# Kernel tuning notes

Measured on AMD Instinct MI355X. Metric: run time of the kernel, lower is better.

## Reference

```python
import jax, jax.numpy as jnp
import numpy as np

H, DK, DV, CHUNK = 4, 256, 256, 32

def _silu(x):
    return x * jax.nn.sigmoid(x)

def _l2norm(x, eps=1e-6):
    return x * jax.lax.rsqrt(jnp.sum(x * x, -1, keepdims=True) + eps)

def _rmsnorm(x, w, eps=1e-5):
    return x * jax.lax.rsqrt(jnp.mean(x * x, -1, keepdims=True) + eps) * w

def _causal_dwconv(x, w):
    # x: (B, L, C), w: (C, K) -> causal depthwise conv -> (B, L, C)
    C = x.shape[-1]
    K = w.shape[-1]
    xp = jnp.pad(x, ((0, 0), (K - 1, 0), (0, 0))).transpose(0, 2, 1)  # NCH
    y = jax.lax.conv_general_dilated(xp, w[:, None, :], (1,), 'VALID',
                                     feature_group_count=C,
                                     dimension_numbers=('NCH', 'OIH', 'NCH'))
    return y.transpose(0, 2, 1)

def _fir(x, filt):
    # x: (B, L, H, D), filt: (H, D, K) depthwise causal FIR per (head, channel)
    B, L, h, d = x.shape
    y = _causal_dwconv(x.reshape(B, L, h * d), filt.reshape(h * d, -1))
    return y.reshape(B, L, h, d)

def _delta_rule_chunkwise(q, k, v, beta):
    # q,k: (B,H,L,DK); v: (B,H,L,DV); beta: (B,H,L). L % CHUNK == 0.
    b, h, L, dk = q.shape
    dv = v.shape[-1]
    n = L // CHUNK
    q = _l2norm(q)
    k = _l2norm(k)
    v = v * beta[..., None]
    k_beta = k * beta[..., None]
    rs = lambda t: t.reshape(b, h, n, CHUNK, -1)
    q, k, v, k_beta = rs(q), rs(k), rs(v), rs(k_beta)
    eye = jnp.eye(CHUNK, dtype=q.dtype)
    strict_lower = jnp.tril(jnp.ones((CHUNK, CHUNK), bool), -1)
    A = jnp.where(strict_lower, jnp.einsum('bhncd,bhnsd->bhncs', k_beta, k), 0.0)
    # The torch row-wise loop computes (I + strict_lower(K_beta K^T))^{-1}
    attn_inv = jax.scipy.linalg.solve_triangular(eye + A, jnp.broadcast_to(eye, A.shape), lower=True)
    u = attn_inv @ v       # (b,h,n,c,dv)
    w = attn_inv @ k_beta  # (b,h,n,c,dk)
    incl_lower = jnp.tril(jnp.ones((CHUNK, CHUNK), bool))

    def step(S, inp):
        q_i, k_i, u_i, w_i = inp
        attn_local = jnp.where(incl_lower, q_i @ jnp.swapaxes(k_i, -1, -2), 0.0)
        u_t = u_i - w_i @ S
        o_i = q_i @ S + attn_local @ u_t
        return S + jnp.swapaxes(k_i, -1, -2) @ u_t, o_i

    S0 = jnp.zeros((b, h, dk, dv), q.dtype)
    xs = tuple(jnp.moveaxis(t, 2, 0) for t in (q, k, u, w))
    S, out = jax.lax.scan(step, S0, xs)
    return jnp.moveaxis(out, 0, 2).reshape(b, h, L, dv), S

def _stats(x):
    # per-branch head statistics over feature dim: mean, var, abs-mean, l2-norm
    return jnp.stack([x.mean(-1), x.var(-1), jnp.abs(x).mean(-1),
                      jnp.sqrt(jnp.sum(x * x, -1))], -1)

def _forward(x, Wq, Wk, Wv, Wb, conv_q, conv_k, conv_v, fir_long, fir_short,
             W1, b1, W2, b2, log_temp, base_bias, conv_residual_logit, rms_w, Wo):
    B, L, D = x.shape
    q = _silu(_causal_dwconv(x @ Wq, conv_q)).reshape(B, L, H, DK)
    k = _silu(_causal_dwconv(x @ Wk, conv_k)).reshape(B, L, H, DK)
    v = _silu(_causal_dwconv(x @ Wv, conv_v)).reshape(B, L, H, DV)
    beta = jax.nn.sigmoid(x @ Wb)  # (B, L, H)
    delta, _S = _delta_rule_chunkwise(q.transpose(0, 2, 1, 3), k.transpose(0, 2, 1, 3),
                                      v.transpose(0, 2, 1, 3), beta.transpose(0, 2, 1))
    delta = delta.transpose(0, 2, 1, 3)  # (B, L, H, DV)
    f_short = _fir(v, fir_short)
    f_long = _fir(v, fir_long)
    stats = jnp.concatenate([_stats(f_short), _stats(f_long), _stats(delta), _stats(v)], -1)
    hidden_exp = jnp.broadcast_to(x[:, :, None, :], (B, L, H, D))
    gate_in = jnp.concatenate([hidden_exp, stats], -1)  # (B,L,H,D+16)
    h1 = jax.nn.gelu(gate_in @ W1 + b1, approximate=False)
    logits = h1 @ W2 + b2 + base_bias  # (B, L, H, 4)
    temp = jax.nn.softplus(log_temp) + 1e-4
    p = jax.nn.softmax(logits / temp[:, None], -1)
    eps = 0.05  # step 0 -> alpha = 1 -> floor = floor_start
    p = jnp.maximum(p, jnp.array([eps, eps, 0.0, 0.0], p.dtype))
    p = p / jnp.sum(p, -1, keepdims=True)
    o = (p[..., 0:1] * f_short + p[..., 1:2] * f_long +
         p[..., 2:3] * delta + p[..., 3:4] * v)
    o = o + 0.5 * jax.nn.sigmoid(conv_residual_logit)[None, None, :, None] * f_short
    o = _rmsnorm(o, rms_w)
    return o.reshape(B, L, H * DV) @ Wo

def setup_inputs():
    key = jax.random.key(0)
    ks = jax.random.split(key, 13)
    B, L, D = 2, 2048, 1024
    f = jnp.float32
    n = lambda k, shape, s=0.02: jax.random.normal(k, shape, f) * s
    return {
        'x': jax.random.normal(ks[0], (B, L, D), f),
        'Wq': n(ks[1], (D, D)),
        'Wk': n(ks[2], (D, D)),
        'Wv': n(ks[3], (D, D)),
        'Wb': n(ks[4], (D, H)),
        'conv_q': n(ks[5], (D, 4), 0.1),
        'conv_k': n(ks[6], (D, 4), 0.1),
        'conv_v': n(ks[7], (D, 4), 0.1),
        'fir_long': n(ks[8], (H, DV, 64)),
        'fir_short': n(ks[9], (H, DV, 5)),
        'W1': n(ks[10], (D + 16, D)),
        'b1': jnp.zeros((D,), f),
        'W2': n(ks[11], (D, 4)),
        'b2': jnp.zeros((4,), f),
        'log_temp': jnp.full((H,), float(np.log(np.expm1(0.7))), f),
        'base_bias': jnp.tile(jnp.array([-0.5, -0.5, 1.0, 3.0], f), (H, 1)),
        'conv_residual_logit': jnp.full((H,), -2.0, f),
        'rms_w': jnp.ones((DV,), f),
        'Wo': n(ks[12], (D, D)),
    }

def reference(x, Wq, Wk, Wv, Wb, conv_q, conv_k, conv_v, fir_long, fir_short,
              W1, b1, W2, b2, log_temp, base_bias, conv_residual_logit, rms_w, Wo):
    return _forward(x, Wq, Wk, Wv, Wb, conv_q, conv_k, conv_v, fir_long, fir_short,
                    W1, b1, W2, b2, log_temp, base_bias, conv_residual_logit, rms_w, Wo)
```

## Files before the change

kernel.cpp:

```cpp
#include <hip/hip_runtime.h>
#include <math.h>

constexpr int NB = 2, NL = 2048, ND = 1024, NH = 4;
constexpr int NCHK = 64;
constexpr int NBL = NB * NL;
#define BLDSZ (NB * NL * ND)

constexpr int OPS_CH = 36864;
constexpr int STG_CH = 26624;

__device__ float g_q[BLDSZ];
__device__ float g_k[BLDSZ];
__device__ float g_v[BLDSZ];
__device__ float g_delta[BLDSZ];
__device__ float g_fs[BLDSZ];
__device__ float g_fl[BLDSZ];
__device__ float g_xw1[BLDSZ];
__device__ float g_beta[NBL * NH];
__device__ unsigned short g_qlb[BLDSZ];
__device__ unsigned short g_klb[BLDSZ];
__device__ unsigned short g_vlb[BLDSZ];
__device__ unsigned short g_ops[(size_t)8 * 64 * OPS_CH];
__device__ unsigned short g_xb[BLDSZ];
__device__ unsigned short g_omixb[BLDSZ];
__device__ unsigned short g_btw[5 * 1024 * 1024];

__device__ __forceinline__ float sigmoidf(float x) { return 1.f / (1.f + expf(-x)); }

__device__ __forceinline__ unsigned short f2bf(float f) {
  union { float f; unsigned int u; } v; v.f = f;
  unsigned int r = v.u + 0x7FFFu + ((v.u >> 16) & 1u);
  return (unsigned short)(r >> 16);
}
__device__ __forceinline__ float bf2f(unsigned int bits16) {
  union { unsigned int u; float f; } v; v.u = bits16 << 16; return v.f;
}
__device__ __forceinline__ unsigned int packbf(float a, float b) {
  return (unsigned int)f2bf(a) | ((unsigned int)f2bf(b) << 16);
}

typedef __attribute__((ext_vector_type(8))) short short8v;
typedef __attribute__((ext_vector_type(16))) float f32x16;

__device__ __forceinline__ unsigned int cvtpk(float lo, float hi) {
  unsigned int r;
  asm("v_cvt_pk_bf16_f32 %0, %1, %2" : "=v"(r) : "v"(lo), "v"(hi));
  return r;
}

__device__ __forceinline__ void mkfrag(const f32x16 v, short8v& fb0, short8v& fb1) {
  unsigned int P0 = cvtpk(v[0], v[1]),   P1 = cvtpk(v[2], v[3]);
  unsigned int P2 = cvtpk(v[4], v[5]),   P3 = cvtpk(v[6], v[7]);
  unsigned int P4 = cvtpk(v[8], v[9]),   P5 = cvtpk(v[10], v[11]);
  unsigned int P6 = cvtpk(v[12], v[13]), P7 = cvtpk(v[14], v[15]);
  asm("v_permlane32_swap_b32 %0, %1" : "+v"(P0), "+v"(P2));
  asm("v_permlane32_swap_b32 %0, %1" : "+v"(P1), "+v"(P3));
  asm("v_permlane32_swap_b32 %0, %1" : "+v"(P4), "+v"(P6));
  asm("v_permlane32_swap_b32 %0, %1" : "+v"(P5), "+v"(P7));
  unsigned int f0[4] = {P0, P1, P2, P3}, f1[4] = {P4, P5, P6, P7};
  fb0 = *(short8v*)f0; fb1 = *(short8v*)f1;
}

#define GLL16(SRC, DST)                                                                    \
  __builtin_amdgcn_global_load_lds(                                                        \
      (const __attribute__((address_space(1))) unsigned int*)(SRC),                        \
      (__attribute__((address_space(3))) unsigned int*)(DST), 16, 0, 0)

__device__ __forceinline__ void gemm128(const unsigned short* __restrict__ A,
                                        const unsigned short* __restrict__ Bt,
                                        float* __restrict__ C, int m0, int n0, int t,
                                        unsigned short* As, unsigned short* Bs) {
  const int w = t >> 6, lane = t & 63, l31 = lane & 31, lhi = lane >> 5;
  const int wm = (w & 1) * 64, wn = (w >> 1) * 64;
  f32x16 acc[2][2];
#pragma unroll
  for (int mt = 0; mt < 2; ++mt)
#pragma unroll
    for (int nt = 0; nt < 2; ++nt)
#pragma unroll
      for (int e = 0; e < 16; ++e) acc[mt][nt][e] = 0.f;

  for (int k0 = 0; k0 < 1024; k0 += 32) {
#pragma unroll
    for (int i = 0; i < 2; ++i) {
      int s0 = i * 256 + w * 64;
      int sl = s0 + lane;
      int srow = sl >> 2, skb = sl & 3;
      GLL16(A + (size_t)(m0 + srow) * 1024 + k0 + skb * 8, &As[s0 * 8]);
      GLL16(Bt + (size_t)(n0 + srow) * 1024 + k0 + skb * 8, &Bs[s0 * 8]);
    }
    __syncthreads();
#pragma unroll
    for (int ksl = 0; ksl < 2; ++ksl) {
      int kb = ksl * 2 + lhi;
      short8v af[2], bf[2];
#pragma unroll
      for (int mt = 0; mt < 2; ++mt) {
        int row = wm + mt * 32 + l31;
        af[mt] = *(const short8v*)&As[row * 32 + kb * 8];
      }
#pragma unroll
      for (int nt = 0; nt < 2; ++nt) {
        int row = wn + nt * 32 + l31;
        bf[nt] = *(const short8v*)&Bs[row * 32 + kb * 8];
      }
#pragma unroll
      for (int mt = 0; mt < 2; ++mt)
#pragma unroll
        for (int nt = 0; nt < 2; ++nt)
          acc[mt][nt] = __builtin_amdgcn_mfma_f32_32x32x16_bf16(af[mt], bf[nt], acc[mt][nt], 0, 0, 0);
    }
    __syncthreads();
  }
#pragma unroll
  for (int mt = 0; mt < 2; ++mt)
#pragma unroll
    for (int nt = 0; nt < 2; ++nt) {
      int col = n0 + wn + nt * 32 + l31;
#pragma unroll
      for (int e = 0; e < 16; ++e) {
        int row = m0 + wm + mt * 32 + (e & 3) + 8 * (e >> 2) + 4 * lhi;
        C[(size_t)row * 1024 + col] = acc[mt][nt][e];
      }
    }
}

__global__ __launch_bounds__(256) void pack_all_kernel(const float* __restrict__ x,
                                                       const float* __restrict__ Wq,
                                                       const float* __restrict__ Wk,
                                                       const float* __restrict__ Wv,
                                                       const float* __restrict__ W1,
                                                       const float* __restrict__ Wo,
                                                       const float* __restrict__ Wb) {
  __shared__ float tile[64][65];
  int blk = blockIdx.x, t = threadIdx.x;
  if (blk < 2048) {
    int i8 = blk * 256 + t;
    const float* p = x + (size_t)i8 * 8;
    float4 a = *(const float4*)p;
    float4 b = *(const float4*)(p + 4);
    uint4 v;
    v.x = packbf(a.x, a.y); v.y = packbf(a.z, a.w);
    v.z = packbf(b.x, b.y); v.w = packbf(b.z, b.w);
    *(uint4*)&g_xb[(size_t)i8 * 8] = v;
    return;
  }
  if (blk < 3328) {
    int sel = (blk - 2048) >> 8, wb = (blk - 2048) & 255;
    const float* W = (sel == 0) ? Wq : (sel == 1) ? Wk : (sel == 2) ? Wv : (sel == 3) ? W1 : Wo;
    int bx = wb & 15, by = wb >> 4;
    int n0 = bx * 64, k0 = by * 64;
#pragma unroll
    for (int i = 0; i < 4; ++i) {
      int id = t + i * 256;
      int r = id >> 4, c4 = (id & 15) * 4;
      float4 v = *(const float4*)&W[(size_t)(k0 + r) * 1024 + n0 + c4];
      tile[r][c4 + 0] = v.x; tile[r][c4 + 1] = v.y; tile[r][c4 + 2] = v.z; tile[r][c4 + 3] = v.w;
    }
    __syncthreads();
    unsigned int* out = (unsigned int*)g_btw + (size_t)sel * 524288;
#pragma unroll
    for (int i = 0; i < 8; ++i) {
      int id = t + i * 256;
      int nn = id >> 5, ku = id & 31;
      out[(size_t)(n0 + nn) * 512 + (k0 >> 1) + ku] = packbf(tile[2 * ku][nn], tile[2 * ku + 1][nn]);
    }
    return;
  }
  int bl = blk - 3328;
  int h = t >> 6, lane = t & 63;
  const float* xr = x + (size_t)bl * ND;
  float acc = 0.f;
  for (int d = lane; d < ND; d += 64) acc += xr[d] * Wb[d * 4 + h];
#pragma unroll
  for (int off = 32; off; off >>= 1) acc += __shfl_xor(acc, off);
  if (lane == 0) g_beta[bl * 4 + h] = sigmoidf(acc);
}

__global__ __launch_bounds__(256) void qkv_gemm_kernel() {
  __shared__ unsigned short As[128 * 32];
  __shared__ unsigned short Bs[128 * 32];
  const int sel = blockIdx.x >> 8, hb = blockIdx.x & 255;
  const unsigned short* A = g_xb;
  const unsigned short* Bt = g_btw + (size_t)sel * 1024 * 1024;
  unsigned short* C = (sel == 0) ? g_qlb : (sel == 1) ? g_klb : g_vlb;
  const int m0 = (hb >> 3) * 128, n0 = (hb & 7) * 128;
  const int t = threadIdx.x;
  const int w = t >> 6, lane = t & 63, l31 = lane & 31, lhi = lane >> 5;
  const int wm = (w & 1) * 64, wn = (w >> 1) * 64;
  f32x16 acc[2][2];
#pragma unroll
  for (int mt = 0; mt < 2; ++mt)
#pragma unroll
    for (int nt = 0; nt < 2; ++nt)
#pragma unroll
      for (int e = 0; e < 16; ++e) acc[mt][nt][e] = 0.f;

  for (int k0 = 0; k0 < 1024; k0 += 32) {
#pragma unroll
    for (int i = 0; i < 2; ++i) {
      int s0 = i * 256 + w * 64;
      int sl = s0 + lane;
      int srow = sl >> 2, skb = sl & 3;
      GLL16(A + (size_t)(m0 + srow) * 1024 + k0 + skb * 8, &As[s0 * 8]);
      GLL16(Bt + (size_t)(n0 + srow) * 1024 + k0 + skb * 8, &Bs[s0 * 8]);
    }
    __syncthreads();
#pragma unroll
    for (int ksl = 0; ksl < 2; ++ksl) {
      int kb = ksl * 2 + lhi;
      short8v af[2], bf[2];
#pragma unroll
      for (int mt = 0; mt < 2; ++mt) {
        int row = wm + mt * 32 + l31;
        af[mt] = *(const short8v*)&As[row * 32 + kb * 8];
      }
#pragma unroll
      for (int nt = 0; nt < 2; ++nt) {
        int row = wn + nt * 32 + l31;
        bf[nt] = *(const short8v*)&Bs[row * 32 + kb * 8];
      }
#pragma unroll
      for (int mt = 0; mt < 2; ++mt)
#pragma unroll
        for (int nt = 0; nt < 2; ++nt)
          acc[mt][nt] = __builtin_amdgcn_mfma_f32_32x32x16_bf16(af[mt], bf[nt], acc[mt][nt], 0, 0, 0);
    }
    __syncthreads();
  }
#pragma unroll
  for (int mt = 0; mt < 2; ++mt)
#pragma unroll
    for (int nt = 0; nt < 2; ++nt) {
      int col = n0 + wn + nt * 32 + l31;
#pragma unroll
      for (int e = 0; e < 16; ++e) {
        int row = m0 + wm + mt * 32 + (e & 3) + 8 * (e >> 2) + 4 * lhi;
        C[(size_t)row * 1024 + col] = f2bf(acc[mt][nt][e]);
      }
    }
}

__global__ __launch_bounds__(256) void conv3_kernel(const float* __restrict__ cq,
                                                    const float* __restrict__ ck,
                                                    const float* __restrict__ cv) {
  int blk = blockIdx.x, t = threadIdx.x;
  int sel = blk >> 14;
  const float* cw = (sel == 0) ? cq : (sel == 1) ? ck : cv;
  const unsigned short* in = (sel == 0) ? g_qlb : (sel == 1) ? g_klb : g_vlb;
  float* out = (sel == 0) ? g_q : (sel == 1) ? g_k : g_v;
  int idx = (blk & 16383) * 256 + t;
  int c = idx & (ND - 1);
  int bl = idx >> 10;
  int l = bl & (NL - 1);
  float w0 = cw[c * 4 + 0], w1 = cw[c * 4 + 1], w2 = cw[c * 4 + 2], w3 = cw[c * 4 + 3];
  float acc = w3 * bf2f(in[(size_t)bl * ND + c]);
  if (l >= 1) acc += w2 * bf2f(in[(size_t)(bl - 1) * ND + c]);
  if (l >= 2) acc += w1 * bf2f(in[(size_t)(bl - 2) * ND + c]);
  if (l >= 3) acc += w0 * bf2f(in[(size_t)(bl - 3) * ND + c]);
  out[idx] = acc * sigmoidf(acc);
}

__global__ __launch_bounds__(256) void hgemm_out_kernel(float* __restrict__ Cext) {
  __shared__ unsigned short As[128 * 32];
  __shared__ unsigned short Bs[128 * 32];
  gemm128(g_omixb, g_btw + (size_t)4 * 1024 * 1024, Cext,
          (blockIdx.x >> 3) * 128, (blockIdx.x & 7) * 128, threadIdx.x, As, Bs);
}

__global__ __launch_bounds__(256) void delta_prep_kernel() {
  __shared__ float X[32][260];
  __shared__ float Y[32][260];
  __shared__ float Am[32][33];
  __shared__ float Tm[32][33];
  __shared__ float bet[32];
  int blk = blockIdx.x;
  int n = blk & 63, h = (blk >> 6) & 3, b = blk >> 8;
  int t = threadIdx.x;
  size_t rowbase = (size_t)(b * NL + n * 32);
  size_t obase = (size_t)blk * OPS_CH;
  const int st_ = t >> 5, j_ = (t >> 4) & 1, lh_ = (t >> 3) & 1, e_ = t & 7;
  const int l31_ = t & 31;

#pragma unroll
  for (int i = 0; i < 8; ++i) {
    int j = t + i * 256;
    int r = j >> 6, d4 = (j & 63) << 2;
    size_t gi = (rowbase + r) * ND + h * 256 + d4;
    *(float4*)&X[r][d4] = *(const float4*)&g_q[gi];
    *(float4*)&Y[r][d4] = *(const float4*)&g_k[gi];
  }
  if (t < 32) bet[t] = g_beta[(rowbase + t) * 4 + h];
  __syncthreads();

  {
    int wv = t >> 6, lane = t & 63;
    int r = wv * 8 + (lane >> 3), sub = lane & 7;
    float sq = 0.f, sk = 0.f;
#pragma unroll
    for (int m4 = 0; m4 < 8; ++m4) {
      float4 a = *(const float4*)&X[r][sub * 32 + m4 * 4];
      float4 bb = *(const float4*)&Y[r][sub * 32 + m4 * 4];
      sq += a.x * a.x + a.y * a.y + a.z * a.z + a.w * a.w;
      sk += bb.x * bb.x + bb.y * bb.y + bb.z * bb.z + bb.w * bb.w;
    }
    sq += __shfl_xor(sq, 1); sq += __shfl_xor(sq, 2); sq += __shfl_xor(sq, 4);
    sk += __shfl_xor(sk, 1); sk += __shfl_xor(sk, 2); sk += __shfl_xor(sk, 4);
    float rq = rsqrtf(sq + 1e-6f), rk = rsqrtf(sk + 1e-6f);
#pragma unroll
    for (int m4 = 0; m4 < 8; ++m4) {
      float4 a = *(const float4*)&X[r][sub * 32 + m4 * 4];
      a.x *= rq; a.y *= rq; a.z *= rq; a.w *= rq;
      *(float4*)&X[r][sub * 32 + m4 * 4] = a;
      float4 bb = *(const float4*)&Y[r][sub * 32 + m4 * 4];
      bb.x *= rk; bb.y *= rk; bb.z *= rk; bb.w *= rk;
      *(float4*)&Y[r][sub * 32 + m4 * 4] = bb;
    }
  }
  __syncthreads();

  if (t < 64) {
    const int al = t & 31, ah = t >> 5;
    f32x16 Cat;
#pragma unroll
    for (int e = 0; e < 16; ++e) Cat[e] = 0.f;
#pragma unroll
    for (int st = 0; st < 16; ++st) {
      int kb = st * 16 + ah * 8;
      float4 a0 = *(const float4*)&X[al][kb], a1 = *(const float4*)&X[al][kb + 4];
      float4 b0 = *(const float4*)&Y[al][kb], b1 = *(const float4*)&Y[al][kb + 4];
      unsigned int af[4] = {cvtpk(a0.x, a0.y), cvtpk(a0.z, a0.w), cvtpk(a1.x, a1.y), cvtpk(a1.z, a1.w)};
      unsigned int bf_[4] = {cvtpk(b0.x, b0.y), cvtpk(b0.z, b0.w), cvtpk(b1.x, b1.y), cvtpk(b1.z, b1.w)};
      Cat = __builtin_amdgcn_mfma_f32_32x32x16_bf16(*(short8v*)af, *(short8v*)bf_, Cat, 0, 0, 0);
    }
#pragma unroll
    for (int e = 0; e < 16; ++e) {
      int row = (e & 3) + 8 * (e >> 2) + 4 * ah, col = al;
      float v = (col <= row) ? Cat[e] : 0.f;
      g_ops[obase + 32768 + (size_t)(((col >> 4) * 64) + ((col >> 3) & 1) * 32 + row) * 8 + (col & 7)] = f2bf(v);
    }
  }

  {
    size_t qb = obase + 8192 + (size_t)(((st_ * 2 + j_) * 64) + lh_ * 32) * 8 + e_;
#pragma unroll 8
    for (int r = 0; r < 32; ++r)
      g_ops[qb + r * 8] = f2bf(X[r][t]);
#pragma unroll
    for (int j = 0; j < 2; ++j)
#pragma unroll
      for (int lh = 0; lh < 2; ++lh) {
        int kr0 = j * 16 + lh * 8;
        uint4 v;
        v.x = packbf(Y[kr0 + 0][t], Y[kr0 + 1][t]);
        v.y = packbf(Y[kr0 + 2][t], Y[kr0 + 3][t]);
        v.z = packbf(Y[kr0 + 4][t], Y[kr0 + 5][t]);
        v.w = packbf(Y[kr0 + 6][t], Y[kr0 + 7][t]);
        *(uint4*)&g_ops[obase + 16384 + (size_t)(((st_ * 2 + j) * 64) + lh * 32 + l31_) * 8] = v;
      }
  }
  __syncthreads();

#pragma unroll
  for (int i = 0; i < 8; ++i) {
    int j = t + i * 256;
    int r = j >> 6, d4 = (j & 63) << 2;
    float be = bet[r];
    float4 bb = *(const float4*)&Y[r][d4];
    bb.x *= be; bb.y *= be; bb.z *= be; bb.w *= be;
    *(float4*)&X[r][d4] = bb;
  }
  __syncthreads();

  if (t < 64) {
    const int al = t & 31, ah = t >> 5;
    f32x16 Cam;
#pragma unroll
    for (int e = 0; e < 16; ++e) Cam[e] = 0.f;
#pragma unroll
    for (int st = 0; st < 16; ++st) {
      int kb = st * 16 + ah * 8;
      float4 a0 = *(const float4*)&X[al][kb], a1 = *(const float4*)&X[al][kb + 4];
      float4 b0 = *(const float4*)&Y[al][kb], b1 = *(const float4*)&Y[al][kb + 4];
      unsigned int af[4] = {cvtpk(a0.x, a0.y), cvtpk(a0.z, a0.w), cvtpk(a1.x, a1.y), cvtpk(a1.z, a1.w)};
      unsigned int bf_[4] = {cvtpk(b0.x, b0.y), cvtpk(b0.z, b0.w), cvtpk(b1.x, b1.y), cvtpk(b1.z, b1.w)};
      Cam = __builtin_amdgcn_mfma_f32_32x32x16_bf16(*(short8v*)af, *(short8v*)bf_, Cam, 0, 0, 0);
    }
#pragma unroll
    for (int e = 0; e < 16; ++e) {
      int row = (e & 3) + 8 * (e >> 2) + 4 * ah, col = al;
      if (col < row) Am[row][col] = Cam[e];
    }
  }
  __syncthreads();

  if (t < 32) {
    const int j = t;
#pragma unroll
    for (int i = 0; i < 32; ++i) {
      float a = (i == j) ? 1.f : 0.f;
#pragma unroll
      for (int m = 0; m < i; ++m) {
        float p = Am[i][m] * Tm[m][j];
        a -= (m >= j) ? p : 0.f;
      }
      Tm[i][j] = a;
    }
  }
  __syncthreads();

  {
    float acc[32];
#pragma unroll
    for (int r = 0; r < 32; ++r) acc[r] = 0.f;
#pragma unroll
    for (int m = 0; m < 32; ++m) {
      float xv = X[m][t];
#pragma unroll
      for (int r = m; r < 32; ++r) acc[r] += Tm[r][m] * xv;
    }
    size_t wb = obase + (size_t)(((st_ * 2 + j_) * 64) + lh_ * 32) * 8 + e_;
#pragma unroll 8
    for (int r = 0; r < 32; ++r)
      g_ops[wb + r * 8] = f2bf(acc[r]);
  }
#pragma unroll
  for (int i = 0; i < 8; ++i) {
    int j = t + i * 256;
    int r = j >> 6, d4 = (j & 63) << 2;
    size_t gi = (rowbase + r) * ND + h * 256 + d4;
    float be = bet[r];
    float4 vv = *(const float4*)&g_v[gi];
    vv.x *= be; vv.y *= be; vv.z *= be; vv.w *= be;
    *(float4*)&Y[r][d4] = vv;
  }
  __syncthreads();

  {
    float acc[32];
#pragma unroll
    for (int r = 0; r < 32; ++r) acc[r] = 0.f;
#pragma unroll
    for (int m = 0; m < 32; ++m) {
      float yv = Y[m][t];
#pragma unroll
      for (int r = m; r < 32; ++r) acc[r] += Tm[r][m] * yv;
    }
    int q = t >> 5;
#pragma unroll
    for (int g = 0; g < 4; ++g)
#pragma unroll
      for (int lh = 0; lh < 2; ++lh) {
        int kr0 = 8 * g + 4 * lh;
        uint2 v;
        v.x = packbf(acc[kr0 + 0], acc[kr0 + 1]);
        v.y = packbf(acc[kr0 + 2], acc[kr0 + 3]);
        *(uint2*)&g_ops[obase + 24576 + (size_t)(((q * 4 + g) * 64) + lh * 32 + l31_) * 4] = v;
      }
  }
}

__global__ __launch_bounds__(256, 1) void scan_fir_kernel(const float* __restrict__ firl,
                                                          const float* __restrict__ firs) {
  __shared__ __align__(16) unsigned char smem[2 * STG_CH * 2];
  const int blk = blockIdx.x;
  const int t = threadIdx.x;

  if (blk < 64) {
    if (t >= 64) return;
    unsigned short (*buf)[STG_CH] = (unsigned short (*)[STG_CH])smem;
    const int bh = blk & 7;
    const int b = bh >> 2, h = bh & 3;
    const int s = blk >> 3;
    const int lane = t;
    const int l31 = lane & 31, lhi = lane >> 5;

    f32x16 Sacc[8];
#pragma unroll
    for (int st = 0; st < 8; ++st)
#pragma unroll
      for (int e = 0; e < 16; ++e) Sacc[st][e] = 0.f;

    const unsigned short* ops = g_ops + (size_t)bh * 64 * OPS_CH;
    const int fo = lane * 8;
    const int utg = 24576 + s * 1024;

#define STAGE_CHUNK(SRC, DST)                                                              \
    {                                                                                      \
      const unsigned short* sp = (SRC);                                                    \
      unsigned short* dp = (DST);                                                          \
      _Pragma("unroll")                                                                    \
      for (int k = 0; k < 48; ++k)                                                         \
        GLL16(sp + (size_t)k * 512 + fo, dp + k * 512);                                    \
      _Pragma("unroll")                                                                    \
      for (int k = 0; k < 2; ++k) {                                                        \
        GLL16(sp + utg + (size_t)k * 512 + fo, dp + 24576 + k * 512);                      \
        GLL16(sp + 32768 + (size_t)k * 512 + fo, dp + 25600 + k * 512);                    \
      }                                                                                    \
    }

    STAGE_CHUNK(ops, &buf[0][0]);

    for (int n = 0; n < 64; ++n) {
      const int cur = n & 1;
      if (n == 0) asm volatile("s_waitcnt vmcnt(0)" ::: "memory");
      else        asm volatile("s_waitcnt vmcnt(16)" ::: "memory");

      if (n < 63) STAGE_CHUNK(ops + (size_t)(n + 1) * OPS_CH, &buf[cur ^ 1][0]);

      const unsigned short* Lb = &buf[cur][0];
      f32x16 wuA, wuB, ooA, ooB;
#pragma unroll
      for (int e = 0; e < 16; ++e) { wuA[e] = 0.f; wuB[e] = 0.f; ooA[e] = 0.f; ooB[e] = 0.f; }

#pragma unroll
      for (int st = 0; st < 8; ++st) {
        short8v s0, s1;
        mkfrag(Sacc[st], s0, s1);
        short8v wa0 = *(const short8v*)&Lb[(st * 2 + 0) * 512 + fo];
        short8v wa1 = *(const short8v*)&Lb[(st * 2 + 1) * 512 + fo];
        short8v qa0 = *(const short8v*)&Lb[8192 + (st * 2 + 0) * 512 + fo];
        short8v qa1 = *(const short8v*)&Lb[8192 + (st * 2 + 1) * 512 + fo];
        wuA = __builtin_amdgcn_mfma_f32_32x32x16_bf16(wa0, s0, wuA, 0, 0, 0);
        wuB = __builtin_amdgcn_mfma_f32_32x32x16_bf16(wa1, s1, wuB, 0, 0, 0);
        ooA = __builtin_amdgcn_mfma_f32_32x32x16_bf16(qa0, s0, ooA, 0, 0, 0);
        ooB = __builtin_amdgcn_mfma_f32_32x32x16_bf16(qa1, s1, ooB, 0, 0, 0);
      }

      f32x16 ut;
#pragma unroll
      for (int g = 0; g < 4; ++g) {
        uint2 uu = *(const uint2*)&Lb[24576 + ((g * 64) + lhi * 32 + l31) * 4];
        ut[4 * g + 0] = bf2f(uu.x & 0xffffu) - wuA[4 * g + 0] - wuB[4 * g + 0];
        ut[4 * g + 1] = bf2f(uu.x >> 16)     - wuA[4 * g + 1] - wuB[4 * g + 1];
        ut[4 * g + 2] = bf2f(uu.y & 0xffffu) - wuA[4 * g + 2] - wuB[4 * g + 2];
        ut[4 * g + 3] = bf2f(uu.y >> 16)     - wuA[4 * g + 3] - wuB[4 * g + 3];
      }
      short8v u0, u1;
      mkfrag(ut, u0, u1);

      {
        short8v aa0 = *(const short8v*)&Lb[25600 + 0 * 512 + fo];
        short8v aa1 = *(const short8v*)&Lb[25600 + 1 * 512 + fo];
        ooA = __builtin_amdgcn_mfma_f32_32x32x16_bf16(aa0, u0, ooA, 0, 0, 0);
        ooB = __builtin_amdgcn_mfma_f32_32x32x16_bf16(aa1, u1, ooB, 0, 0, 0);
      }
#pragma unroll
      for (int st = 0; st < 8; ++st) {
        short8v ka0 = *(const short8v*)&Lb[16384 + (st * 2 + 0) * 512 + fo];
        short8v ka1 = *(const short8v*)&Lb[16384 + (st * 2 + 1) * 512 + fo];
        Sacc[st] = __builtin_amdgcn_mfma_f32_32x32x16_bf16(ka0, u0, Sacc[st], 0, 0, 0);
        Sacc[st] = __builtin_amdgcn_mfma_f32_32x32x16_bf16(ka1, u1, Sacc[st], 0, 0, 0);
      }

      size_t ob = ((size_t)(b * NL + n * 32)) * ND + h * 256 + s * 32 + l31;
#pragma unroll
      for (int e = 0; e < 16; ++e) {
        int row = (e & 3) + 8 * (e >> 2) + 4 * lhi;
        g_delta[ob + (size_t)row * ND] = ooA[e] + ooB[e];
      }
    }
#undef STAGE_CHUNK
  } else if (blk < 64 + 512) {
    float (*ft)[257] = (float (*)[257])smem;
    int fb_ = blk - 64;
    int cbk = fb_ & 3, lb = (fb_ >> 2) & 63, b = fb_ >> 8;
    int c = cbk * 256 + t;
    const float* fbp = firl + (size_t)cbk * 256 * 64;
#pragma unroll 4
    for (int i = 0; i < 64; ++i) {
      int j = t + i * 256;
      ft[j & 63][j >> 6] = fbp[j];
    }
    __syncthreads();
    float ff[64];
#pragma unroll
    for (int i = 0; i < 64; ++i) ff[i] = ft[i][t];
    float acc[32];
#pragma unroll
    for (int i = 0; i < 32; ++i) acc[i] = 0.f;
    const float* vb = g_v + (size_t)b * NL * ND + c;
    const int l0 = lb * 32;
#pragma unroll
    for (int d = 0; d < 95; ++d) {
      int lr = l0 - 63 + d;
      float vv = (lr >= 0) ? vb[(size_t)lr * ND] : 0.f;
      const int lo = (d > 63) ? (d - 63) : 0;
      const int hi = (d < 31) ? d : 31;
#pragma unroll
      for (int li = lo; li <= hi; ++li) acc[li] += ff[d - li] * vv;
    }
    float* ob = g_fl + ((size_t)(b * NL + l0)) * ND + c;
#pragma unroll
    for (int li = 0; li < 32; ++li) ob[(size_t)li * ND] = acc[li];
  } else if (blk < 64 + 512 + BLDSZ / 1024) {
    int idx4 = (blk - 576) * 256 + t;
    int c4 = idx4 & 255;
    int bl = idx4 >> 8;
    int l = bl & (NL - 1);
    float fw[4][5];
#pragma unroll
    for (int j = 0; j < 4; ++j)
#pragma unroll
      for (int tap = 0; tap < 5; ++tap) fw[j][tap] = firs[(c4 * 4 + j) * 5 + tap];
    float4 acc = {0.f, 0.f, 0.f, 0.f};
    const float4* v4 = (const float4*)g_v;
#pragma unroll
    for (int tap = 0; tap < 5; ++tap) {
      int ls = l + tap - 4;
      if (ls >= 0) {
        float4 vv = v4[(size_t)(bl + tap - 4) * 256 + c4];
        acc.x += fw[0][tap] * vv.x; acc.y += fw[1][tap] * vv.y;
        acc.z += fw[2][tap] * vv.z; acc.w += fw[3][tap] * vv.w;
      }
    }
    ((float4*)g_fs)[(size_t)bl * 256 + c4] = acc;
  } else {
    unsigned short* As = (unsigned short*)smem;
    unsigned short* Bs = (unsigned short*)smem + 4096;
    int hb = blk - (64 + 512 + BLDSZ / 1024);
    gemm128(g_xb, g_btw + (size_t)3 * 1024 * 1024, g_xw1,
            (hb >> 3) * 128, (hb & 7) * 128, t, As, Bs);
  }
}

__global__ __launch_bounds__(256) void tail_kernel(const float* __restrict__ W1,
                                                   const float* __restrict__ b1,
                                                   const float* __restrict__ W2,
                                                   const float* __restrict__ b2,
                                                   const float* __restrict__ log_temp,
                                                   const float* __restrict__ base_bias,
                                                   const float* __restrict__ crl,
                                                   const float* __restrict__ rms_w) {
  __shared__ float st[4][16];
  __shared__ float red[4][4];
  __shared__ float pl[4][4];
  int bl = blockIdx.x, t = threadIdx.x;
  int h = t >> 6, lane = t & 63;

  {
    size_t base = (size_t)bl * ND + h * 256 + lane * 4;
#pragma unroll
    for (int br = 0; br < 4; ++br) {
      const float* p = (br == 0) ? g_fs : (br == 1) ? g_fl : (br == 2) ? g_delta : g_v;
      float4 x4 = *(const float4*)&p[base];
      float s = x4.x + x4.y + x4.z + x4.w;
      float s2 = x4.x * x4.x + x4.y * x4.y + x4.z * x4.z + x4.w * x4.w;
      float sa = fabsf(x4.x) + fabsf(x4.y) + fabsf(x4.z) + fabsf(x4.w);
#pragma unroll
      for (int off = 32; off; off >>= 1) {
        s += __shfl_xor(s, off);
        s2 += __shfl_xor(s2, off);
        sa += __shfl_xor(sa, off);
      }
      if (lane == 0) {
        float mean = s * (1.f / 256.f);
        st[h][br * 4 + 0] = mean;
        st[h][br * 4 + 1] = s2 * (1.f / 256.f) - mean * mean;
        st[h][br * 4 + 2] = sa * (1.f / 256.f);
        st[h][br * 4 + 3] = sqrtf(s2);
      }
    }
  }
  __syncthreads();

  const float* W1s = W1 + 1024 * 1024;
  for (int hh = 0; hh < 4; ++hh) {
    float sv[16];
#pragma unroll
    for (int s = 0; s < 16; ++s) sv[s] = st[hh][s];
    float a0 = 0.f, a1 = 0.f, a2 = 0.f, a3 = 0.f;
    for (int j = t; j < 1024; j += 256) {
      float val = g_xw1[(size_t)bl * 1024 + j] + b1[j];
#pragma unroll
      for (int s = 0; s < 16; ++s) val += sv[s] * W1s[s * 1024 + j];
      float gg = 0.5f * val * (1.f + erff(val * 0.70710678118654752f));
      float4 w2 = *(const float4*)&W2[j * 4];
      a0 += gg * w2.x; a1 += gg * w2.y; a2 += gg * w2.z; a3 += gg * w2.w;
    }
#pragma unroll
    for (int off = 32; off; off >>= 1) {
      a0 += __shfl_xor(a0, off); a1 += __shfl_xor(a1, off);
      a2 += __shfl_xor(a2, off); a3 += __shfl_xor(a3, off);
    }
    if (lane == 0) { red[h][0] = a0; red[h][1] = a1; red[h][2] = a2; red[h][3] = a3; }
    __syncthreads();
    if (t == 0) {
      float lg[4];
#pragma unroll
      for (int m = 0; m < 4; ++m)
        lg[m] = red[0][m] + red[1][m] + red[2][m] + red[3][m] + b2[m] + base_bias[hh * 4 + m];
      float lt = log_temp[hh];
      float sp = (lt > 20.f) ? lt : log1pf(expf(lt));
      float inv = 1.f / (sp + 1e-4f);
      float z0 = lg[0] * inv, z1 = lg[1] * inv, z2 = lg[2] * inv, z3 = lg[3] * inv;
      float mx = fmaxf(fmaxf(z0, z1), fmaxf(z2, z3));
      float e0 = expf(z0 - mx), e1 = expf(z1 - mx), e2 = expf(z2 - mx), e3 = expf(z3 - mx);
      float si = 1.f / (e0 + e1 + e2 + e3);
      float p0 = e0 * si, p1 = e1 * si, p2 = e2 * si, p3 = e3 * si;
      p0 = fmaxf(p0, 0.05f); p1 = fmaxf(p1, 0.05f);
      float s2i = 1.f / (p0 + p1 + p2 + p3);
      p0 *= s2i; p1 *= s2i; p2 *= s2i; p3 *= s2i;
      p0 += 0.5f * sigmoidf(crl[hh]);
      pl[hh][0] = p0; pl[hh][1] = p1; pl[hh][2] = p2; pl[hh][3] = p3;
    }
    __syncthreads();
  }

  float p0 = pl[h][0], p1 = pl[h][1], p2 = pl[h][2], p3 = pl[h][3];
  size_t base = (size_t)bl * ND + h * 256 + lane * 4;
  float4 a = *(const float4*)&g_fs[base];
  float4 bb = *(const float4*)&g_fl[base];
  float4 c = *(const float4*)&g_delta[base];
  float4 d = *(const float4*)&g_v[base];
  float o0 = p0 * a.x + p1 * bb.x + p2 * c.x + p3 * d.x;
  float o1 = p0 * a.y + p1 * bb.y + p2 * c.y + p3 * d.y;
  float o2 = p0 * a.z + p1 * bb.z + p2 * c.z + p3 * d.z;
  float o3 = p0 * a.w + p1 * bb.w + p2 * c.w + p3 * d.w;
  float s2 = o0 * o0 + o1 * o1 + o2 * o2 + o3 * o3;
#pragma unroll
  for (int off = 32; off; off >>= 1) s2 += __shfl_xor(s2, off);
  float rms = rsqrtf(s2 * (1.f / 256.f) + 1e-5f);
  float4 w4 = *(const float4*)&rms_w[lane * 4];
  uint2 pw;
  pw.x = packbf(o0 * rms * w4.x, o1 * rms * w4.y);
  pw.y = packbf(o2 * rms * w4.z, o3 * rms * w4.w);
  *(uint2*)&g_omixb[base] = pw;
}

extern "C" void kernel_launch(void* const* d_in, const int* in_sizes, int n_in,
                              void* d_out, int out_size, void* d_ws, size_t ws_size,
                              hipStream_t stream) {
  const float* x = (const float*)d_in[0];
  const float* Wq = (const float*)d_in[1];
  const float* Wk = (const float*)d_in[2];
  const float* Wv = (const float*)d_in[3];
  const float* Wb = (const float*)d_in[4];
  const float* cq = (const float*)d_in[5];
  const float* ck = (const float*)d_in[6];
  const float* cv = (const float*)d_in[7];
  const float* firl = (const float*)d_in[8];
  const float* firs = (const float*)d_in[9];
  const float* W1 = (const float*)d_in[10];
  const float* b1 = (const float*)d_in[11];
  const float* W2 = (const float*)d_in[12];
  const float* b2 = (const float*)d_in[13];
  const float* ltp = (const float*)d_in[14];
  const float* bbs = (const float*)d_in[15];
  const float* crl = (const float*)d_in[16];
  const float* rw = (const float*)d_in[17];
  const float* Wo = (const float*)d_in[18];
  float* out = (float*)d_out;

  dim3 blk(256);
  pack_all_kernel<<<2048 + 5 * 256 + NBL, blk, 0, stream>>>(x, Wq, Wk, Wv, W1, Wo, Wb);
  qkv_gemm_kernel<<<768, blk, 0, stream>>>();
  conv3_kernel<<<3 * 16384, blk, 0, stream>>>(cq, ck, cv);
  delta_prep_kernel<<<NB * NH * NCHK, blk, 0, stream>>>();
  scan_fir_kernel<<<64 + 512 + BLDSZ / 1024 + 256, blk, 0, stream>>>(firl, firs);
  tail_kernel<<<NBL, blk, 0, stream>>>(W1, b1, W2, b2, ltp, bbs, crl, rw);
  hgemm_out_kernel<<<256, blk, 0, stream>>>(out);
}
```

Before: 438.4 us.

## Fuse q/k causal conv into delta prep and widen GEMM k-tile with swizzle

The causal depthwise conv plus SiLU for q and k now runs inside delta_prep_kernel, reading the bf16 projections directly. This removes the fp32 g_q/g_k intermediates and two thirds of the conv kernel's traffic. Separately, the shared GEMM core moves to a 64-wide k-tile with an XOR-swizzled LDS layout, halving the barriers per k-step and reducing bank conflicts. The larger LDS footprint (32KB per block) may lower occupancy, and the scan kernel's smem must be large enough to hold it.

```diff
diff --git a/kernel.cpp b/kernel.cpp
--- a/kernel.cpp
+++ b/kernel.cpp
@@ -9,8 +9,6 @@
 constexpr int OPS_CH = 36864;
 constexpr int STG_CH = 26624;
 
-__device__ float g_q[BLDSZ];
-__device__ float g_k[BLDSZ];
 __device__ float g_v[BLDSZ];
 __device__ float g_delta[BLDSZ];
 __device__ float g_fs[BLDSZ];
@@ -66,13 +64,13 @@
       (const __attribute__((address_space(1))) unsigned int*)(SRC),                        \
       (__attribute__((address_space(3))) unsigned int*)(DST), 16, 0, 0)
 
-__device__ __forceinline__ void gemm128(const unsigned short* __restrict__ A,
-                                        const unsigned short* __restrict__ Bt,
-                                        float* __restrict__ C, int m0, int n0, int t,
-                                        unsigned short* As, unsigned short* Bs) {
+__device__ __forceinline__ void gemm128_core(const unsigned short* __restrict__ A,
+                                             const unsigned short* __restrict__ Bt,
+                                             int m0, int n0, int t,
+                                             unsigned short* As, unsigned short* Bs,
+                                             f32x16 acc[2][2]) {
   const int w = t >> 6, lane = t & 63, l31 = lane & 31, lhi = lane >> 5;
   const int wm = (w & 1) * 64, wn = (w >> 1) * 64;
-  f32x16 acc[2][2];
 #pragma unroll
   for (int mt = 0; mt < 2; ++mt)
 #pragma unroll
@@ -80,29 +78,29 @@
 #pragma unroll
       for (int e = 0; e < 16; ++e) acc[mt][nt][e] = 0.f;
 
-  for (int k0 = 0; k0 < 1024; k0 += 32) {
-#pragma unroll
-    for (int i = 0; i < 2; ++i) {
-      int s0 = i * 256 + w * 64;
-      int sl = s0 + lane;
-      int srow = sl >> 2, skb = sl & 3;
-      GLL16(A + (size_t)(m0 + srow) * 1024 + k0 + skb * 8, &As[s0 * 8]);
-      GLL16(Bt + (size_t)(n0 + srow) * 1024 + k0 + skb * 8, &Bs[s0 * 8]);
+  for (int k0 = 0; k0 < 1024; k0 += 64) {
+#pragma unroll
+    for (int i = 0; i < 4; ++i) {
+      int sl = i * 4 + w;
+      int srow = sl * 8 + (lane >> 3);
+      int gc = (((lane & 7) ^ (srow & 7))) * 8;
+      GLL16(A + (size_t)(m0 + srow) * 1024 + k0 + gc, &As[sl * 512]);
+      GLL16(Bt + (size_t)(n0 + srow) * 1024 + k0 + gc, &Bs[sl * 512]);
     }
     __syncthreads();
 #pragma unroll
-    for (int ksl = 0; ksl < 2; ++ksl) {
+    for (int ksl = 0; ksl < 4; ++ksl) {
       int kb = ksl * 2 + lhi;
       short8v af[2], bf[2];
 #pragma unroll
       for (int mt = 0; mt < 2; ++mt) {
         int row = wm + mt * 32 + l31;
-        af[mt] = *(const short8v*)&As[row * 32 + kb * 8];
+        af[mt] = *(const short8v*)&As[row * 64 + ((kb ^ (row & 7)) * 8)];
       }
 #pragma unroll
       for (int nt = 0; nt < 2; ++nt) {
         int row = wn + nt * 32 + l31;
-        bf[nt] = *(const short8v*)&Bs[row * 32 + kb * 8];
+        bf[nt] = *(const short8v*)&Bs[row * 64 + ((kb ^ (row & 7)) * 8)];
       }
 #pragma unroll
       for (int mt = 0; mt < 2; ++mt)
@@ -112,17 +110,6 @@
     }
     __syncthreads();
   }
-#pragma unroll
-  for (int mt = 0; mt < 2; ++mt)
-#pragma unroll
-    for (int nt = 0; nt < 2; ++nt) {
-      int col = n0 + wn + nt * 32 + l31;
-#pragma unroll
-      for (int e = 0; e < 16; ++e) {
-        int row = m0 + wm + mt * 32 + (e & 3) + 8 * (e >> 2) + 4 * lhi;
-        C[(size_t)row * 1024 + col] = acc[mt][nt][e];
-      }
-    }
 }
 
 __global__ __launch_bounds__(256) void pack_all_kernel(const float* __restrict__ x,
@@ -178,10 +165,9 @@
 }
 
 __global__ __launch_bounds__(256) void qkv_gemm_kernel() {
-  __shared__ unsigned short As[128 * 32];
-  __shared__ unsigned short Bs[128 * 32];
+  __shared__ unsigned short As[128 * 64];
+  __shared__ unsigned short Bs[128 * 64];
   const int sel = blockIdx.x >> 8, hb = blockIdx.x & 255;
-  const unsigned short* A = g_xb;
   const unsigned short* Bt = g_btw + (size_t)sel * 1024 * 1024;
   unsigned short* C = (sel == 0) ? g_qlb : (sel == 1) ? g_klb : g_vlb;
   const int m0 = (hb >> 3) * 128, n0 = (hb & 7) * 128;
@@ -189,45 +175,7 @@
   const int w = t >> 6, lane = t & 63, l31 = lane & 31, lhi = lane >> 5;
   const int wm = (w & 1) * 64, wn = (w >> 1) * 64;
   f32x16 acc[2][2];
-#pragma unroll
-  for (int mt = 0; mt < 2; ++mt)
-#pragma unroll
-    for (int nt = 0; nt < 2; ++nt)
-#pragma unroll
-      for (int e = 0; e < 16; ++e) acc[mt][nt][e] = 0.f;
-
-  for (int k0 = 0; k0 < 1024; k0 += 32) {
-#pragma unroll
-    for (int i = 0; i < 2; ++i) {
-      int s0 = i * 256 + w * 64;
-      int sl = s0 + lane;
-      int srow = sl >> 2, skb = sl & 3;
-      GLL16(A + (size_t)(m0 + srow) * 1024 + k0 + skb * 8, &As[s0 * 8]);
-      GLL16(Bt + (size_t)(n0 + srow) * 1024 + k0 + skb * 8, &Bs[s0 * 8]);
-    }
-    __syncthreads();
-#pragma unroll
-    for (int ksl = 0; ksl < 2; ++ksl) {
-      int kb = ksl * 2 + lhi;
-      short8v af[2], bf[2];
-#pragma unroll
-      for (int mt = 0; mt < 2; ++mt) {
-        int row = wm + mt * 32 + l31;
-        af[mt] = *(const short8v*)&As[row * 32 + kb * 8];
-      }
-#pragma unroll
-      for (int nt = 0; nt < 2; ++nt) {
-        int row = wn + nt * 32 + l31;
-        bf[nt] = *(const short8v*)&Bs[row * 32 + kb * 8];
-      }
-#pragma unroll
-      for (int mt = 0; mt < 2; ++mt)
-#pragma unroll
-        for (int nt = 0; nt < 2; ++nt)
-          acc[mt][nt] = __builtin_amdgcn_mfma_f32_32x32x16_bf16(af[mt], bf[nt], acc[mt][nt], 0, 0, 0);
-    }
-    __syncthreads();
-  }
+  gemm128_core(g_xb, Bt, m0, n0, t, As, Bs, acc);
 #pragma unroll
   for (int mt = 0; mt < 2; ++mt)
 #pragma unroll
@@ -241,34 +189,44 @@
     }
 }
 
-__global__ __launch_bounds__(256) void conv3_kernel(const float* __restrict__ cq,
-                                                    const float* __restrict__ ck,
-                                                    const float* __restrict__ cv) {
+__global__ __launch_bounds__(256) void convv_kernel(const float* __restrict__ cv) {
   int blk = blockIdx.x, t = threadIdx.x;
-  int sel = blk >> 14;
-  const float* cw = (sel == 0) ? cq : (sel == 1) ? ck : cv;
-  const unsigned short* in = (sel == 0) ? g_qlb : (sel == 1) ? g_klb : g_vlb;
-  float* out = (sel == 0) ? g_q : (sel == 1) ? g_k : g_v;
-  int idx = (blk & 16383) * 256 + t;
+  int idx = blk * 256 + t;
   int c = idx & (ND - 1);
   int bl = idx >> 10;
   int l = bl & (NL - 1);
-  float w0 = cw[c * 4 + 0], w1 = cw[c * 4 + 1], w2 = cw[c * 4 + 2], w3 = cw[c * 4 + 3];
-  float acc = w3 * bf2f(in[(size_t)bl * ND + c]);
-  if (l >= 1) acc += w2 * bf2f(in[(size_t)(bl - 1) * ND + c]);
-  if (l >= 2) acc += w1 * bf2f(in[(size_t)(bl - 2) * ND + c]);
-  if (l >= 3) acc += w0 * bf2f(in[(size_t)(bl - 3) * ND + c]);
-  out[idx] = acc * sigmoidf(acc);
+  float w0 = cv[c * 4 + 0], w1 = cv[c * 4 + 1], w2 = cv[c * 4 + 2], w3 = cv[c * 4 + 3];
+  float acc = w3 * bf2f(g_vlb[(size_t)bl * ND + c]);
+  if (l >= 1) acc += w2 * bf2f(g_vlb[(size_t)(bl - 1) * ND + c]);
+  if (l >= 2) acc += w1 * bf2f(g_vlb[(size_t)(bl - 2) * ND + c]);
+  if (l >= 3) acc += w0 * bf2f(g_vlb[(size_t)(bl - 3) * ND + c]);
+  g_v[idx] = acc * sigmoidf(acc);
 }
 
 __global__ __launch_bounds__(256) void hgemm_out_kernel(float* __restrict__ Cext) {
-  __shared__ unsigned short As[128 * 32];
-  __shared__ unsigned short Bs[128 * 32];
-  gemm128(g_omixb, g_btw + (size_t)4 * 1024 * 1024, Cext,
-          (blockIdx.x >> 3) * 128, (blockIdx.x & 7) * 128, threadIdx.x, As, Bs);
-}
-
-__global__ __launch_bounds__(256) void delta_prep_kernel() {
+  __shared__ unsigned short As[128 * 64];
+  __shared__ unsigned short Bs[128 * 64];
+  const int m0 = (blockIdx.x >> 3) * 128, n0 = (blockIdx.x & 7) * 128;
+  const int t = threadIdx.x;
+  const int w = t >> 6, lane = t & 63, l31 = lane & 31, lhi = lane >> 5;
+  const int wm = (w & 1) * 64, wn = (w >> 1) * 64;
+  f32x16 acc[2][2];
+  gemm128_core(g_omixb, g_btw + (size_t)4 * 1024 * 1024, m0, n0, t, As, Bs, acc);
+#pragma unroll
+  for (int mt = 0; mt < 2; ++mt)
+#pragma unroll
+    for (int nt = 0; nt < 2; ++nt) {
+      int col = n0 + wn + nt * 32 + l31;
+#pragma unroll
+      for (int e = 0; e < 16; ++e) {
+        int row = m0 + wm + mt * 32 + (e & 3) + 8 * (e >> 2) + 4 * lhi;
+        Cext[(size_t)row * 1024 + col] = acc[mt][nt][e];
+      }
+    }
+}
+
+__global__ __launch_bounds__(256) void delta_prep_kernel(const float* __restrict__ cq,
+                                                         const float* __restrict__ ck) {
   __shared__ float X[32][260];
   __shared__ float Y[32][260];
   __shared__ float Am[32][33];
@@ -282,13 +240,28 @@
   const int st_ = t >> 5, j_ = (t >> 4) & 1, lh_ = (t >> 3) & 1, e_ = t & 7;
   const int l31_ = t & 31;
 
-#pragma unroll
-  for (int i = 0; i < 8; ++i) {
-    int j = t + i * 256;
-    int r = j >> 6, d4 = (j & 63) << 2;
-    size_t gi = (rowbase + r) * ND + h * 256 + d4;
-    *(float4*)&X[r][d4] = *(const float4*)&g_q[gi];
-    *(float4*)&Y[r][d4] = *(const float4*)&g_k[gi];
+  {
+    const int hcol = h * 256 + t;
+    const unsigned short* qp = g_qlb + hcol;
+    const unsigned short* kp = g_klb + hcol;
+    float wq0 = cq[hcol * 4 + 0], wq1 = cq[hcol * 4 + 1], wq2 = cq[hcol * 4 + 2], wq3 = cq[hcol * 4 + 3];
+    float wk0 = ck[hcol * 4 + 0], wk1 = ck[hcol * 4 + 1], wk2 = ck[hcol * 4 + 2], wk3 = ck[hcol * 4 + 3];
+    float qa = 0.f, qb_ = 0.f, qc = 0.f, ka = 0.f, kb_ = 0.f, kc = 0.f;
+    if (n > 0) {
+      qa = bf2f(qp[(rowbase - 3) * 1024]); qb_ = bf2f(qp[(rowbase - 2) * 1024]); qc = bf2f(qp[(rowbase - 1) * 1024]);
+      ka = bf2f(kp[(rowbase - 3) * 1024]); kb_ = bf2f(kp[(rowbase - 2) * 1024]); kc = bf2f(kp[(rowbase - 1) * 1024]);
+    }
+#pragma unroll 4
+    for (int r = 0; r < 32; ++r) {
+      float qd = bf2f(qp[(rowbase + r) * 1024]);
+      float kd = bf2f(kp[(rowbase + r) * 1024]);
+      float aq = wq3 * qd + wq2 * qc + wq1 * qb_ + wq0 * qa;
+      float ak = wk3 * kd + wk2 * kc + wk1 * kb_ + wk0 * ka;
+      X[r][t] = aq * sigmoidf(aq);
+      Y[r][t] = ak * sigmoidf(ak);
+      qa = qb_; qb_ = qc; qc = qd;
+      ka = kb_; kb_ = kc; kc = kd;
+    }
   }
   if (t < 32) bet[t] = g_beta[(rowbase + t) * 4 + h];
   __syncthreads();
@@ -617,10 +590,24 @@
     ((float4*)g_fs)[(size_t)bl * 256 + c4] = acc;
   } else {
     unsigned short* As = (unsigned short*)smem;
-    unsigned short* Bs = (unsigned short*)smem + 4096;
+    unsigned short* Bs = (unsigned short*)smem + 8192;
     int hb = blk - (64 + 512 + BLDSZ / 1024);
-    gemm128(g_xb, g_btw + (size_t)3 * 1024 * 1024, g_xw1,
-            (hb >> 3) * 128, (hb & 7) * 128, t, As, Bs);
+    const int m0 = (hb >> 3) * 128, n0 = (hb & 7) * 128;
+    const int w = t >> 6, lane = t & 63, l31 = lane & 31, lhi = lane >> 5;
+    const int wm = (w & 1) * 64, wn = (w >> 1) * 64;
+    f32x16 acc[2][2];
+    gemm128_core(g_xb, g_btw + (size_t)3 * 1024 * 1024, m0, n0, t, As, Bs, acc);
+#pragma unroll
+    for (int mt = 0; mt < 2; ++mt)
+#pragma unroll
+      for (int nt = 0; nt < 2; ++nt) {
+        int col = n0 + wn + nt * 32 + l31;
+#pragma unroll
+        for (int e = 0; e < 16; ++e) {
+          int row = m0 + wm + mt * 32 + (e & 3) + 8 * (e >> 2) + 4 * lhi;
+          g_xw1[(size_t)row * 1024 + col] = acc[mt][nt][e];
+        }
+      }
   }
 }
 
@@ -755,8 +742,8 @@
   dim3 blk(256);
   pack_all_kernel<<<2048 + 5 * 256 + NBL, blk, 0, stream>>>(x, Wq, Wk, Wv, W1, Wo, Wb);
   qkv_gemm_kernel<<<768, blk, 0, stream>>>();
-  conv3_kernel<<<3 * 16384, blk, 0, stream>>>(cq, ck, cv);
-  delta_prep_kernel<<<NB * NH * NCHK, blk, 0, stream>>>();
+  convv_kernel<<<16384, blk, 0, stream>>>(cv);
+  delta_prep_kernel<<<NB * NH * NCHK, blk, 0, stream>>>(cq, ck);
   scan_fir_kernel<<<64 + 512 + BLDSZ / 1024 + 256, blk, 0, stream>>>(firl, firs);
   tail_kernel<<<NBL, blk, 0, stream>>>(W1, b1, W2, b2, ltp, bbs, crl, rw);
   hgemm_out_kernel<<<256, blk, 0, stream>>>(out);
```

Result: faster. 386.8 us (-11.8%).
